# Kernel tuning notes

Hardware: AMD Instinct MI355X
Metric: run time of the kernel (lower is better)

Reference implementation:

```python
import jax, jax.numpy as jnp
import numpy as np

N_NODES = 100000
N_EDGES = 1600000
N_RELS = 8
IN_F, HID_F, OUT_F = 64, 64, 32


def rgcn_conv(x, src, dst, etype, W, root, bias, num_nodes, num_rels):
    """PyG RGCNConv: out[i] = x[i]@root + bias + sum_r mean_{j in N_r(i)} x[j]@W_r."""
    E = src.shape[0]
    seg = dst * num_rels + etype  # combined (node, relation) segment id
    cnt = jax.ops.segment_sum(jnp.ones((E,), x.dtype), seg,
                              num_segments=num_nodes * num_rels)
    norm = 1.0 / jnp.maximum(cnt[seg], 1.0)  # per-edge 1/|N_r(dst)|
    h = jnp.einsum('ni,rio->rno', x, W)      # [R, N, O] relation-transformed feats
    msg = h[etype, src] * norm[:, None]      # gather per edge, normalize
    agg = jax.ops.segment_sum(msg, dst, num_segments=num_nodes)
    return agg + x @ root + bias


def setup_inputs() -> dict:
    key = jax.random.key(0)
    ks = jax.random.split(key, 10)
    x = jax.random.normal(ks[0], (N_NODES, IN_F), dtype=jnp.float32)
    edge_index = jax.random.randint(ks[1], (2, N_EDGES), 0, N_NODES, dtype=jnp.int64)
    edge_type = jax.random.randint(ks[2], (N_EDGES,), 0, N_RELS, dtype=jnp.int64)
    s1 = 1.0 / np.sqrt(IN_F)
    s2 = 1.0 / np.sqrt(HID_F)
    W1 = jax.random.uniform(ks[3], (N_RELS, IN_F, HID_F), jnp.float32, -s1, s1)
    root1 = jax.random.uniform(ks[4], (IN_F, HID_F), jnp.float32, -s1, s1)
    b1 = jnp.zeros((HID_F,), jnp.float32)
    W2 = jax.random.uniform(ks[5], (N_RELS, HID_F, OUT_F), jnp.float32, -s2, s2)
    root2 = jax.random.uniform(ks[6], (HID_F, OUT_F), jnp.float32, -s2, s2)
    b2 = jnp.zeros((OUT_F,), jnp.float32)
    return {"x": x, "edge_index": edge_index, "edge_type": edge_type,
            "W1": W1, "root1": root1, "b1": b1,
            "W2": W2, "root2": root2, "b2": b2}


def reference(x, edge_index, edge_type, W1, root1, b1, W2, root2, b2):
    src, dst = edge_index[0], edge_index[1]
    h = rgcn_conv(x, src, dst, edge_type, W1, root1, b1, N_NODES, N_RELS)
    h = jax.nn.relu(h)
    out = rgcn_conv(h, src, dst, edge_type, W2, root2, b2, N_NODES, N_RELS)
    return out
```

## Files before the change

### kernel.cpp

```cpp
#include <hip/hip_runtime.h>
#include <hip/hip_bf16.h>

#define N_NODES 100000
#define N_EDGES 1600000
#define N_RELS  8
#define IN_F    64
#define HID_F   64
#define OUT_F   32
#define NSEG    (N_NODES * N_RELS)
#define SCAN_EPB 1024
#define SCAN_NB  ((NSEG + SCAN_EPB - 1) / SCAN_EPB)

typedef __attribute__((ext_vector_type(8))) short short8;
typedef __attribute__((ext_vector_type(4))) float f32x4;

__device__ __forceinline__ float b2f(unsigned short u) {
    return __uint_as_float(((unsigned)u) << 16);
}
__device__ __forceinline__ unsigned short f2b(float f) {
    unsigned u = __float_as_uint(f);
    u += 0x7FFFu + ((u >> 16) & 1u);
    return (unsigned short)(u >> 16);
}

__global__ void k_hist(const int* __restrict__ dst, const int* __restrict__ et,
                       int* __restrict__ cnt, int* __restrict__ rank) {
    int e = blockIdx.x * blockDim.x + threadIdx.x;
    if (e < N_EDGES) {
        int seg = dst[e] * N_RELS + et[e];
        rank[e] = atomicAdd(&cnt[seg], 1);
    }
}

__global__ void k_scanA(const int* __restrict__ cnt, int* __restrict__ bsums) {
    __shared__ int red[256];
    int t = threadIdx.x;
    int base = blockIdx.x * SCAN_EPB + t * 4;
    int s = 0;
    #pragma unroll
    for (int j = 0; j < 4; ++j) {
        int idx = base + j;
        if (idx < NSEG) s += cnt[idx];
    }
    red[t] = s;
    __syncthreads();
    for (int st = 128; st > 0; st >>= 1) {
        if (t < st) red[t] += red[t + st];
        __syncthreads();
    }
    if (t == 0) bsums[blockIdx.x] = red[0];
}

__global__ void k_scanC(const int* __restrict__ cnt, const int* __restrict__ bsums,
                        int* __restrict__ offs) {
    __shared__ int red[256];
    __shared__ int ts[256];
    int t = threadIdx.x;

    int partial = 0;
    #pragma unroll
    for (int jj = 0; jj < 4; ++jj) {
        int j = t + jj * 256;
        if (j < SCAN_NB && j < blockIdx.x) partial += bsums[j];
    }
    red[t] = partial;
    __syncthreads();
    for (int st = 128; st > 0; st >>= 1) {
        if (t < st) red[t] += red[t + st];
        __syncthreads();
    }
    const int base0 = red[0];

    int base = blockIdx.x * SCAN_EPB + t * 4;
    int v[4];
    int local = 0;
    #pragma unroll
    for (int j = 0; j < 4; ++j) {
        int idx = base + j;
        v[j] = (idx < NSEG) ? cnt[idx] : 0;
        local += v[j];
    }
    ts[t] = local;
    __syncthreads();
    for (int off = 1; off < 256; off <<= 1) {
        int x = (t >= off) ? ts[t - off] : 0;
        __syncthreads();
        ts[t] += x;
        __syncthreads();
    }
    int run = base0 + (ts[t] - local);
    #pragma unroll
    for (int j = 0; j < 4; ++j) {
        int idx = base + j;
        if (idx < NSEG) offs[idx] = run;
        run += v[j];
    }
}

#define PREP_W1 (576 * 64)
#define PREP_W2 (576 * 32)
#define PREP_CVT (N_NODES * 64 / 4)
#define PREP_TOT (PREP_W1 + PREP_W2 + PREP_CVT)
__global__ void k_scat_prep(const int* __restrict__ src, const int* __restrict__ dst,
                            const int* __restrict__ et, const int* __restrict__ offs,
                            const int* __restrict__ rank, int* __restrict__ ssrc,
                            const float* __restrict__ W1, const float* __restrict__ root1,
                            const float* __restrict__ W2, const float* __restrict__ root2,
                            const float* __restrict__ x,
                            ushort* __restrict__ Wt1b, ushort* __restrict__ Wt2b,
                            ushort* __restrict__ xb) {
    int idx = blockIdx.x * 256 + threadIdx.x;
    if (idx < N_EDGES) {
        int r = et[idx];
        int seg = dst[idx] * N_RELS + r;
        ssrc[offs[seg] + rank[idx]] = src[idx] * 16 + r;
    } else {
        int j = idx - N_EDGES;
        if (j < PREP_W1) {
            int o = j / 576, k = j - o * 576;
            float v = (k < 512) ? W1[k * 64 + o] : root1[(k - 512) * 64 + o];
            Wt1b[j] = f2b(v);
        } else if (j < PREP_W1 + PREP_W2) {
            int j2 = j - PREP_W1;
            int o = j2 / 576, k = j2 - o * 576;
            float v = (k < 512) ? W2[k * 32 + o] : root2[(k - 512) * 32 + o];
            Wt2b[j2] = f2b(v);
        } else {
            int j2 = j - PREP_W1 - PREP_W2;
            if (j2 < PREP_CVT) {
                float4 v = *(const float4*)(x + j2 * 4);
                ushort4 u;
                u.x = f2b(v.x); u.y = f2b(v.y); u.z = f2b(v.z); u.w = f2b(v.w);
                *(ushort4*)(xb + j2 * 4) = u;
            }
        }
    }
}

template <int NOUT, bool RELU, typename OutT>
__global__ __launch_bounds__(512, 4) void k_layer(
        const ushort* __restrict__ xb, const int* __restrict__ offs,
        const int* __restrict__ cnt, const int* __restrict__ ssrc,
        const ushort* __restrict__ Wtb, const float* __restrict__ bias,
        OutT* __restrict__ out) {
    constexpr int NT = NOUT / 16;
    constexpr int S  = 8 / NT;
    __shared__ __align__(16) ushort A_lds[16][584];
    __shared__ f32x4 pc[6][64];

    const int tid = threadIdx.x;
    const int w = tid >> 6;
    const int f = tid & 63;
    const int node0 = blockIdx.x * 16;

    const int t = w % NT, q = w / NT;
    constexpr int cbase = 18 / S, crem = 18 % S;
    const int cs = q * cbase + (q < crem ? q : crem);
    const int ce = cs + cbase + (q < crem ? 1 : 0);
    const int n0 = t * 16;
    const ushort* bptr = Wtb + (n0 + (f & 15)) * 576 + ((f >> 4) * 8);
    short8 bcur = *(const short8*)(bptr + cs * 32);

    int ov = 0, cv = 0;
    if (f < 16) {
        ov = offs[(node0 + w * 2) * N_RELS + f];
        cv = cnt [(node0 + w * 2) * N_RELS + f];
    }

    for (int nd = 0; nd < 2; ++nd) {
        const int m = w * 2 + nd;
        const int node = node0 + m;
        const int s0 = __builtin_amdgcn_readlane(ov, nd * 8);
        const int ct = __builtin_amdgcn_readlane(ov, nd * 8 + 7)
                     + __builtin_amdgcn_readlane(cv, nd * 8 + 7) - s0;

        float a[8];
        #pragma unroll
        for (int r = 0; r < 8; ++r) a[r] = 0.0f;

        for (int cb = 0; cb < ct; cb += 64) {
            int n = ct - cb;
            if (n > 64) n = 64;
            int pk = 15;
            if (f < n) pk = ssrc[s0 + cb + f];
            for (int e = 0; e < n; e += 16) {
                int pv[16];
                float xv[16];
                #pragma unroll
                for (int i = 0; i < 16; ++i)
                    pv[i] = __builtin_amdgcn_readlane(pk, e + i);
                #pragma unroll
                for (int i = 0; i < 16; ++i)
                    xv[i] = b2f(xb[(size_t)(pv[i] >> 4) * 64 + f]);
                #pragma unroll
                for (int i = 0; i < 16; ++i) {
                    const int rl = pv[i] & 15;
                    if (rl < 4) {
                        if (rl < 2) { if (rl == 0) a[0] += xv[i]; else a[1] += xv[i]; }
                        else        { if (rl == 2) a[2] += xv[i]; else a[3] += xv[i]; }
                    } else if (rl < 8) {
                        if (rl < 6) { if (rl == 4) a[4] += xv[i]; else a[5] += xv[i]; }
                        else        { if (rl == 6) a[6] += xv[i]; else a[7] += xv[i]; }
                    }
                }
            }
        }

        #pragma unroll
        for (int r = 0; r < 8; ++r) {
            int c = __builtin_amdgcn_readlane(cv, nd * 8 + r);
            float inv = 1.0f / (float)(c > 0 ? c : 1);
            A_lds[m][r * 64 + f] = f2b(a[r] * inv);
        }
        A_lds[m][512 + f] = xb[node * 64 + f];
    }
    __syncthreads();

    f32x4 acc = (f32x4){0.0f, 0.0f, 0.0f, 0.0f};
    const ushort* aptr = &A_lds[f & 15][(f >> 4) * 8];
    for (int c = cs; c < ce; ++c) {
        short8 bnext = bcur;
        if (c + 1 < ce) bnext = *(const short8*)(bptr + (c + 1) * 32);
        short8 af = *(const short8*)(aptr + c * 32);
        acc = __builtin_amdgcn_mfma_f32_16x16x32_bf16(af, bcur, acc, 0, 0, 0);
        bcur = bnext;
    }

    if (q > 0) pc[w - NT][f] = acc;
    __syncthreads();
    if (q == 0) {
        #pragma unroll
        for (int j = 1; j < S; ++j) {
            f32x4 p = pc[t + NT * (j - 1)][f];
            acc.x += p.x; acc.y += p.y; acc.z += p.z; acc.w += p.w;
        }
        const int col = f & 15;
        const float bs = bias[n0 + col];
        const int mrow = (f >> 4) * 4;
        #pragma unroll
        for (int i = 0; i < 4; ++i) {
            float v = acc[i] + bs;
            if (RELU) v = fmaxf(v, 0.0f);
            size_t oi = (size_t)(node0 + mrow + i) * NOUT + n0 + col;
            if constexpr (sizeof(OutT) == 2) out[oi] = (OutT)f2b(v);
            else                             out[oi] = (OutT)v;
        }
    }
}

extern "C" void kernel_launch(void* const* d_in, const int* in_sizes, int n_in,
                              void* d_out, int out_size, void* d_ws, size_t ws_size,
                              hipStream_t stream) {
    const float* x     = (const float*)d_in[0];
    const int*   ei    = (const int*)d_in[1];
    const int*   et    = (const int*)d_in[2];
    const float* W1    = (const float*)d_in[3];
    const float* root1 = (const float*)d_in[4];
    const float* b1    = (const float*)d_in[5];
    const float* W2    = (const float*)d_in[6];
    const float* root2 = (const float*)d_in[7];
    const float* b2    = (const float*)d_in[8];
    float* out = (float*)d_out;

    const int* src = ei;
    const int* dst = ei + N_EDGES;

    char* ws = (char*)d_ws;
    int*    cnt   = (int*)(ws);
    int*    offs  = (int*)(ws + (size_t)NSEG * 4);
    int*    bsums = (int*)(ws + (size_t)NSEG * 8);
    int*    ssrc  = (int*)(ws + (size_t)NSEG * 8 + 4096);
    ushort* xb    = (ushort*)(ws + (size_t)NSEG * 8 + 4096 + (size_t)N_EDGES * 4);
    ushort* h1b   = (ushort*)((char*)xb + (size_t)N_NODES * 64 * 2);
    int*    rank  = (int*)h1b;
    ushort* Wt1b  = (ushort*)((char*)h1b + (size_t)N_NODES * 64 * 2);
    ushort* Wt2b  = (ushort*)((char*)Wt1b + (size_t)PREP_W1 * 2);

    hipMemsetAsync(cnt, 0, (size_t)NSEG * 4, stream);

    int eb = (N_EDGES + 255) / 256;
    k_hist<<<eb, 256, 0, stream>>>(dst, et, cnt, rank);
    k_scanA<<<SCAN_NB, 256, 0, stream>>>(cnt, bsums);
    k_scanC<<<SCAN_NB, 256, 0, stream>>>(cnt, bsums, offs);

    int spb = (N_EDGES + PREP_TOT + 255) / 256;
    k_scat_prep<<<spb, 256, 0, stream>>>(src, dst, et, offs, rank, ssrc,
                                         W1, root1, W2, root2, x,
                                         Wt1b, Wt2b, xb);

    k_layer<64, true, ushort><<<N_NODES / 16, 512, 0, stream>>>(
        xb, offs, cnt, ssrc, Wt1b, b1, h1b);
    k_layer<32, false, float><<<N_NODES / 16, 512, 0, stream>>>(
        h1b, offs, cnt, ssrc, Wt2b, b2, out);
}
```

Measured before the change: 441.0 us.

## Balance edge aggregation across warps using LDS float atomics per block

Each block's 16 destination nodes have their edges pooled, and all 8 warps take 32-edge chunks of the pool instead of each warp handling its own two nodes. Results are accumulated with float atomicAdd into an fp32 LDS tile, and the sorted source index is packed with the local destination row so each edge knows its target. Mean normalization moves into the MFMA A-operand load, which scales and converts to bf16 there. This is meant to remove load imbalance from warps with high-degree nodes, at the cost of LDS atomic contention, doubled LDS footprint and extra conversion work in the inner GEMM loop.

New measurement: 1.302 ms. 195% more time.

```diff
diff --git a/kernel.cpp b/kernel.cpp
--- a/kernel.cpp
+++ b/kernel.cpp
@@ -112,8 +112,9 @@
     int idx = blockIdx.x * 256 + threadIdx.x;
     if (idx < N_EDGES) {
         int r = et[idx];
-        int seg = dst[idx] * N_RELS + r;
-        ssrc[offs[seg] + rank[idx]] = src[idx] * 16 + r;
+        int d = dst[idx];
+        int seg = d * N_RELS + r;
+        ssrc[offs[seg] + rank[idx]] = src[idx] * 256 + (d & 15) * 16 + r;
     } else {
         int j = idx - N_EDGES;
         if (j < PREP_W1) {
@@ -137,6 +138,7 @@
     }
 }
 
+#define AST 584
 template <int NOUT, bool RELU, typename OutT>
 __global__ __launch_bounds__(512, 4) void k_layer(
         const ushort* __restrict__ xb, const int* __restrict__ offs,
@@ -145,8 +147,10 @@
         OutT* __restrict__ out) {
     constexpr int NT = NOUT / 16;
     constexpr int S  = 8 / NT;
-    __shared__ __align__(16) ushort A_lds[16][584];
-    __shared__ f32x4 pc[6][64];
+    __shared__ __align__(16) float smem_f[16 * AST + 192];
+    float* Af   = smem_f;
+    float* invp = smem_f + 16 * AST;
+    f32x4* pc   = (f32x4*)smem_f;
 
     const int tid = threadIdx.x;
     const int w = tid >> 6;
@@ -161,77 +165,80 @@
     const ushort* bptr = Wtb + (n0 + (f & 15)) * 576 + ((f >> 4) * 8);
     short8 bcur = *(const short8*)(bptr + cs * 32);
 
-    int ov = 0, cv = 0;
-    if (f < 16) {
-        ov = offs[(node0 + w * 2) * N_RELS + f];
-        cv = cnt [(node0 + w * 2) * N_RELS + f];
-    }
-
-    for (int nd = 0; nd < 2; ++nd) {
-        const int m = w * 2 + nd;
-        const int node = node0 + m;
-        const int s0 = __builtin_amdgcn_readlane(ov, nd * 8);
-        const int ct = __builtin_amdgcn_readlane(ov, nd * 8 + 7)
-                     + __builtin_amdgcn_readlane(cv, nd * 8 + 7) - s0;
-
-        float a[8];
-        #pragma unroll
-        for (int r = 0; r < 8; ++r) a[r] = 0.0f;
-
-        for (int cb = 0; cb < ct; cb += 64) {
-            int n = ct - cb;
-            if (n > 64) n = 64;
-            int pk = 15;
-            if (f < n) pk = ssrc[s0 + cb + f];
-            for (int e = 0; e < n; e += 16) {
-                int pv[16];
-                float xv[16];
-                #pragma unroll
-                for (int i = 0; i < 16; ++i)
-                    pv[i] = __builtin_amdgcn_readlane(pk, e + i);
-                #pragma unroll
-                for (int i = 0; i < 16; ++i)
-                    xv[i] = b2f(xb[(size_t)(pv[i] >> 4) * 64 + f]);
-                #pragma unroll
-                for (int i = 0; i < 16; ++i) {
-                    const int rl = pv[i] & 15;
-                    if (rl < 4) {
-                        if (rl < 2) { if (rl == 0) a[0] += xv[i]; else a[1] += xv[i]; }
-                        else        { if (rl == 2) a[2] += xv[i]; else a[3] += xv[i]; }
-                    } else if (rl < 8) {
-                        if (rl < 6) { if (rl == 4) a[4] += xv[i]; else a[5] += xv[i]; }
-                        else        { if (rl == 6) a[6] += xv[i]; else a[7] += xv[i]; }
-                    }
+    #pragma unroll
+    for (int i = 0; i < 5; ++i) {
+        int j = tid + i * 512;
+        if (j < (16 * AST) / 4) ((float4*)Af)[j] = make_float4(0.f, 0.f, 0.f, 0.f);
+    }
+    if (tid < 128) {
+        int c = cnt[node0 * N_RELS + tid];
+        invp[(tid >> 3) * 12 + (tid & 7)] = 1.0f / (float)(c > 0 ? c : 1);
+    } else if (tid < 144) {
+        invp[(tid - 128) * 12 + 8] = 1.0f;
+    }
+    __syncthreads();
+
+    Af[(w * 2) * AST + 512 + f]     = b2f(xb[(size_t)(node0 + w * 2) * 64 + f]);
+    Af[(w * 2 + 1) * AST + 512 + f] = b2f(xb[(size_t)(node0 + w * 2 + 1) * 64 + f]);
+
+    const int bstart = offs[node0 * N_RELS];
+    const int bend = (node0 + 16 < N_NODES) ? offs[(node0 + 16) * N_RELS] : N_EDGES;
+    const int ntot = bend - bstart;
+
+    for (int base = w * 32; base < ntot; base += 256) {
+        int n = ntot - base;
+        if (n > 32) n = 32;
+        int pk = 15;
+        if (f < n) pk = ssrc[bstart + base + f];
+        for (int e = 0; e < n; e += 16) {
+            int pv[16];
+            ushort uv[16];
+            #pragma unroll
+            for (int i = 0; i < 16; ++i)
+                pv[i] = __builtin_amdgcn_readlane(pk, e + i);
+            #pragma unroll
+            for (int i = 0; i < 16; ++i)
+                uv[i] = xb[(size_t)((unsigned)pv[i] >> 8) * 64 + f];
+            #pragma unroll
+            for (int i = 0; i < 16; ++i) {
+                const int rl = pv[i] & 15;
+                if (rl < 8) {
+                    const int m = (pv[i] >> 4) & 15;
+                    atomicAdd(&Af[m * AST + rl * 64 + f], b2f(uv[i]));
                 }
             }
         }
-
-        #pragma unroll
-        for (int r = 0; r < 8; ++r) {
-            int c = __builtin_amdgcn_readlane(cv, nd * 8 + r);
-            float inv = 1.0f / (float)(c > 0 ? c : 1);
-            A_lds[m][r * 64 + f] = f2b(a[r] * inv);
-        }
-        A_lds[m][512 + f] = xb[node * 64 + f];
     }
     __syncthreads();
 
     f32x4 acc = (f32x4){0.0f, 0.0f, 0.0f, 0.0f};
-    const ushort* aptr = &A_lds[f & 15][(f >> 4) * 8];
+    const int m15 = f & 15;
+    const int q8 = (f >> 4) * 8;
+    const float* arow = Af + m15 * AST;
+    const float* ivrow = invp + m15 * 12;
     for (int c = cs; c < ce; ++c) {
         short8 bnext = bcur;
         if (c + 1 < ce) bnext = *(const short8*)(bptr + (c + 1) * 32);
-        short8 af = *(const short8*)(aptr + c * 32);
+        const int k0 = c * 32 + q8;
+        float4 u0 = *(const float4*)(arow + k0);
+        float4 u1 = *(const float4*)(arow + k0 + 4);
+        const float iv = ivrow[k0 >> 6];
+        short8 af;
+        af[0] = (short)f2b(u0.x * iv); af[1] = (short)f2b(u0.y * iv);
+        af[2] = (short)f2b(u0.z * iv); af[3] = (short)f2b(u0.w * iv);
+        af[4] = (short)f2b(u1.x * iv); af[5] = (short)f2b(u1.y * iv);
+        af[6] = (short)f2b(u1.z * iv); af[7] = (short)f2b(u1.w * iv);
         acc = __builtin_amdgcn_mfma_f32_16x16x32_bf16(af, bcur, acc, 0, 0, 0);
         bcur = bnext;
     }
-
-    if (q > 0) pc[w - NT][f] = acc;
+    __syncthreads();
+
+    if (q > 0) pc[(w - NT) * 64 + f] = acc;
     __syncthreads();
     if (q == 0) {
         #pragma unroll
         for (int j = 1; j < S; ++j) {
-            f32x4 p = pc[t + NT * (j - 1)][f];
+            f32x4 p = pc[(t + NT * (j - 1)) * 64 + f];
             acc.x += p.x; acc.y += p.y; acc.z += p.z; acc.w += p.w;
         }
         const int col = f & 15;
```

## Fuse count, scan and scatter preprocessing into one cooperative kernel

Applied to the files above, without the earlier changes.

Replaces the memset and four preprocessing launches (histogram, two scan passes, scatter/weight prep) with a single cooperative kernel. It uses grid-stride loops over 1024 blocks, with grid.sync between phases. The aim is to remove kernel launch and inter-kernel gaps. In exchange it adds grid-wide barriers and runs the atomic and scatter phases with fewer resident threads than the original one-thread-per-edge launches.

Measured after the change: 869.1 us. 1.97x slower.

```diff
diff --git a/kernel.cpp b/kernel.cpp
--- a/kernel.cpp
+++ b/kernel.cpp
@@ -1,5 +1,8 @@
 #include <hip/hip_runtime.h>
 #include <hip/hip_bf16.h>
+#include <hip/hip_cooperative_groups.h>
+
+namespace cg = cooperative_groups;
 
 #define N_NODES 100000
 #define N_EDGES 1600000
@@ -10,6 +13,7 @@
 #define NSEG    (N_NODES * N_RELS)
 #define SCAN_EPB 1024
 #define SCAN_NB  ((NSEG + SCAN_EPB - 1) / SCAN_EPB)
+#define PRE_BLOCKS 1024
 
 typedef __attribute__((ext_vector_type(8))) short short8;
 typedef __attribute__((ext_vector_type(4))) float f32x4;
@@ -23,99 +27,30 @@
     return (unsigned short)(u >> 16);
 }
 
-__global__ void k_hist(const int* __restrict__ dst, const int* __restrict__ et,
-                       int* __restrict__ cnt, int* __restrict__ rank) {
-    int e = blockIdx.x * blockDim.x + threadIdx.x;
-    if (e < N_EDGES) {
-        int seg = dst[e] * N_RELS + et[e];
-        rank[e] = atomicAdd(&cnt[seg], 1);
-    }
-}
-
-__global__ void k_scanA(const int* __restrict__ cnt, int* __restrict__ bsums) {
-    __shared__ int red[256];
-    int t = threadIdx.x;
-    int base = blockIdx.x * SCAN_EPB + t * 4;
-    int s = 0;
-    #pragma unroll
-    for (int j = 0; j < 4; ++j) {
-        int idx = base + j;
-        if (idx < NSEG) s += cnt[idx];
-    }
-    red[t] = s;
-    __syncthreads();
-    for (int st = 128; st > 0; st >>= 1) {
-        if (t < st) red[t] += red[t + st];
-        __syncthreads();
-    }
-    if (t == 0) bsums[blockIdx.x] = red[0];
-}
-
-__global__ void k_scanC(const int* __restrict__ cnt, const int* __restrict__ bsums,
-                        int* __restrict__ offs) {
-    __shared__ int red[256];
-    __shared__ int ts[256];
-    int t = threadIdx.x;
-
-    int partial = 0;
-    #pragma unroll
-    for (int jj = 0; jj < 4; ++jj) {
-        int j = t + jj * 256;
-        if (j < SCAN_NB && j < blockIdx.x) partial += bsums[j];
-    }
-    red[t] = partial;
-    __syncthreads();
-    for (int st = 128; st > 0; st >>= 1) {
-        if (t < st) red[t] += red[t + st];
-        __syncthreads();
-    }
-    const int base0 = red[0];
-
-    int base = blockIdx.x * SCAN_EPB + t * 4;
-    int v[4];
-    int local = 0;
-    #pragma unroll
-    for (int j = 0; j < 4; ++j) {
-        int idx = base + j;
-        v[j] = (idx < NSEG) ? cnt[idx] : 0;
-        local += v[j];
-    }
-    ts[t] = local;
-    __syncthreads();
-    for (int off = 1; off < 256; off <<= 1) {
-        int x = (t >= off) ? ts[t - off] : 0;
-        __syncthreads();
-        ts[t] += x;
-        __syncthreads();
-    }
-    int run = base0 + (ts[t] - local);
-    #pragma unroll
-    for (int j = 0; j < 4; ++j) {
-        int idx = base + j;
-        if (idx < NSEG) offs[idx] = run;
-        run += v[j];
-    }
-}
-
 #define PREP_W1 (576 * 64)
 #define PREP_W2 (576 * 32)
 #define PREP_CVT (N_NODES * 64 / 4)
 #define PREP_TOT (PREP_W1 + PREP_W2 + PREP_CVT)
-__global__ void k_scat_prep(const int* __restrict__ src, const int* __restrict__ dst,
-                            const int* __restrict__ et, const int* __restrict__ offs,
-                            const int* __restrict__ rank, int* __restrict__ ssrc,
-                            const float* __restrict__ W1, const float* __restrict__ root1,
-                            const float* __restrict__ W2, const float* __restrict__ root2,
-                            const float* __restrict__ x,
-                            ushort* __restrict__ Wt1b, ushort* __restrict__ Wt2b,
-                            ushort* __restrict__ xb) {
-    int idx = blockIdx.x * 256 + threadIdx.x;
-    if (idx < N_EDGES) {
-        int r = et[idx];
-        int seg = dst[idx] * N_RELS + r;
-        ssrc[offs[seg] + rank[idx]] = src[idx] * 16 + r;
-    } else {
-        int j = idx - N_EDGES;
+
+__global__ void __launch_bounds__(256, 8) k_pre(
+        const int* __restrict__ src, const int* __restrict__ dst,
+        const int* __restrict__ et,
+        int* __restrict__ cnt, int* __restrict__ rank, int* __restrict__ offs,
+        int* __restrict__ bsums, int* __restrict__ ssrc,
+        const float* __restrict__ W1, const float* __restrict__ root1,
+        const float* __restrict__ W2, const float* __restrict__ root2,
+        const float* __restrict__ x,
+        ushort* __restrict__ Wt1b, ushort* __restrict__ Wt2b,
+        ushort* __restrict__ xb) {
+    cg::grid_group grid = cg::this_grid();
+    __shared__ int red[256];
+    __shared__ int ts[256];
+    const int t = threadIdx.x;
+    const int gtid = blockIdx.x * 256 + t;
+    const int gsz = gridDim.x * 256;
+
+    for (int i = gtid; i < NSEG; i += gsz) cnt[i] = 0;
+    for (int j = gtid; j < PREP_TOT; j += gsz) {
         if (j < PREP_W1) {
             int o = j / 576, k = j - o * 576;
             float v = (k < 512) ? W1[k * 64 + o] : root1[(k - 512) * 64 + o];
@@ -127,13 +62,85 @@
             Wt2b[j2] = f2b(v);
         } else {
             int j2 = j - PREP_W1 - PREP_W2;
-            if (j2 < PREP_CVT) {
-                float4 v = *(const float4*)(x + j2 * 4);
-                ushort4 u;
-                u.x = f2b(v.x); u.y = f2b(v.y); u.z = f2b(v.z); u.w = f2b(v.w);
-                *(ushort4*)(xb + j2 * 4) = u;
-            }
-        }
+            float4 v = *(const float4*)(x + (size_t)j2 * 4);
+            ushort4 u;
+            u.x = f2b(v.x); u.y = f2b(v.y); u.z = f2b(v.z); u.w = f2b(v.w);
+            *(ushort4*)(xb + (size_t)j2 * 4) = u;
+        }
+    }
+    grid.sync();
+
+    for (int e = gtid; e < N_EDGES; e += gsz) {
+        int r = et[e];
+        int seg = dst[e] * N_RELS + r;
+        rank[e] = atomicAdd(&cnt[seg], 1);
+    }
+    grid.sync();
+
+    if (blockIdx.x < SCAN_NB) {
+        int base = blockIdx.x * SCAN_EPB + t * 4;
+        int s = 0;
+        #pragma unroll
+        for (int j = 0; j < 4; ++j) {
+            int idx = base + j;
+            if (idx < NSEG) s += cnt[idx];
+        }
+        red[t] = s;
+        __syncthreads();
+        for (int st = 128; st > 0; st >>= 1) {
+            if (t < st) red[t] += red[t + st];
+            __syncthreads();
+        }
+        if (t == 0) bsums[blockIdx.x] = red[0];
+    }
+    grid.sync();
+
+    if (blockIdx.x < SCAN_NB) {
+        int partial = 0;
+        #pragma unroll
+        for (int jj = 0; jj < 4; ++jj) {
+            int j = t + jj * 256;
+            if (j < SCAN_NB && j < (int)blockIdx.x) partial += bsums[j];
+        }
+        red[t] = partial;
+        __syncthreads();
+        for (int st = 128; st > 0; st >>= 1) {
+            if (t < st) red[t] += red[t + st];
+            __syncthreads();
+        }
+        const int base0 = red[0];
+
+        int base = blockIdx.x * SCAN_EPB + t * 4;
+        int v[4];
+        int local = 0;
+        #pragma unroll
+        for (int j = 0; j < 4; ++j) {
+            int idx = base + j;
+            v[j] = (idx < NSEG) ? cnt[idx] : 0;
+            local += v[j];
+        }
+        ts[t] = local;
+        __syncthreads();
+        for (int off = 1; off < 256; off <<= 1) {
+            int xv = (t >= off) ? ts[t - off] : 0;
+            __syncthreads();
+            ts[t] += xv;
+            __syncthreads();
+        }
+        int run = base0 + (ts[t] - local);
+        #pragma unroll
+        for (int j = 0; j < 4; ++j) {
+            int idx = base + j;
+            if (idx < NSEG) offs[idx] = run;
+            run += v[j];
+        }
+    }
+    grid.sync();
+
+    for (int e = gtid; e < N_EDGES; e += gsz) {
+        int r = et[e];
+        int seg = dst[e] * N_RELS + r;
+        ssrc[offs[seg] + rank[e]] = src[e] * 16 + r;
     }
 }
 
@@ -276,17 +283,14 @@
     ushort* Wt1b  = (ushort*)((char*)h1b + (size_t)N_NODES * 64 * 2);
     ushort* Wt2b  = (ushort*)((char*)Wt1b + (size_t)PREP_W1 * 2);
 
-    hipMemsetAsync(cnt, 0, (size_t)NSEG * 4, stream);
-
-    int eb = (N_EDGES + 255) / 256;
-    k_hist<<<eb, 256, 0, stream>>>(dst, et, cnt, rank);
-    k_scanA<<<SCAN_NB, 256, 0, stream>>>(cnt, bsums);
-    k_scanC<<<SCAN_NB, 256, 0, stream>>>(cnt, bsums, offs);
-
-    int spb = (N_EDGES + PREP_TOT + 255) / 256;
-    k_scat_prep<<<spb, 256, 0, stream>>>(src, dst, et, offs, rank, ssrc,
-                                         W1, root1, W2, root2, x,
-                                         Wt1b, Wt2b, xb);
+    void* args[] = {
+        (void*)&src, (void*)&dst, (void*)&et,
+        (void*)&cnt, (void*)&rank, (void*)&offs, (void*)&bsums, (void*)&ssrc,
+        (void*)&W1, (void*)&root1, (void*)&W2, (void*)&root2, (void*)&x,
+        (void*)&Wt1b, (void*)&Wt2b, (void*)&xb
+    };
+    hipLaunchCooperativeKernel((void*)k_pre, dim3(PRE_BLOCKS), dim3(256),
+                               args, 0, stream);
 
     k_layer<64, true, ushort><<<N_NODES / 16, 512, 0, stream>>>(
         xb, offs, cnt, ssrc, Wt1b, b1, h1b);
```
